# Performance work log

Measured on AMD Instinct MI355X. Metric: run time of the kernel, lower is better.

The kernel has to match this reference:

```python
import jax, jax.numpy as jnp
import numpy as np
from jax import lax

D = 30   # embedding_dim (hardcoded in repo)
Q = 30   # question length
N = 4000 # number of sentences in doc
S = 100  # tokens per sentence
K = 5    # k_for_maxpool
SLOPE = 0.1  # LeakyReLU negative slope


def setup_inputs() -> dict:
    key = jax.random.key(0)
    ks = jax.random.split(key, 20)
    rn = lambda k, sh: jax.random.normal(k, sh, dtype=jnp.float32)
    ru = lambda k, sh: jax.random.uniform(k, sh, dtype=jnp.float32)
    return {
        "doc_sents_embeds": rn(ks[0], (N, S, D)),
        "sents_gaf": ru(ks[1], (N, 3)),
        "question_embeds": rn(ks[2], (Q, D)),
        "q_idfs": ru(ks[3], (Q, 1)),
        "doc_gaf": ru(ks[4], (4,)),
        "conv1_w": rn(ks[5], (D, D, 3)) * 0.1,
        "conv1_b": rn(ks[6], (D,)) * 0.1,
        "conv2_w": rn(ks[7], (D, D, 3)) * 0.1,
        "conv2_b": rn(ks[8], (D,)) * 0.1,
        "qw_W": rn(ks[9], (1, D + 1)) * 0.1,
        "qw_b": rn(ks[10], (1,)) * 0.1,
        "lq1_W": rn(ks[11], (8, 6)) * 0.1,
        "lq1_b": rn(ks[12], (8,)) * 0.1,
        "lq2_W": rn(ks[13], (1, 8)) * 0.1,
        "lq2_b": rn(ks[14], (1,)) * 0.1,
        "so_W": rn(ks[15], (1, 4)) * 0.1,
        "so_b": rn(ks[16], (1,)) * 0.1,
        "fl_W": rn(ks[17], (1, 5)) * 0.1,
        "fl_b": rn(ks[18], (1,)) * 0.1,
    }


def _leaky(x):
    return jnp.where(x >= 0, x, SLOPE * x)


def _conv_block(x, w, b):
    # x: [B, L, D]. torch Conv1d(D, D, 3, padding=2) then slice [1:L+1]
    # is exactly a 'same' conv with padding 1 on each side; then residual add.
    y = lax.conv_general_dilated(x.transpose(0, 2, 1), w, (1,), [(1, 1)],
                                 dimension_numbers=("NCH", "OIH", "NCH"))
    y = _leaky(y + b[None, :, None])
    return y.transpose(0, 2, 1) + x


def _cos_sim(A, B):
    # A: [Q, D], B: [N, S, D] -> [N, Q, S] (num/den as in torch my_cosine_sim)
    num = jnp.einsum("qd,nsd->nqs", A, B)
    den = jnp.linalg.norm(A, axis=-1)[None, :, None] * jnp.linalg.norm(B, axis=-1)[:, None, :]
    return num / den


def _pool(sim):
    # sort-based k-max pooling -> [max, avg_of_top_k]; sim: [N, Q, S] -> [N, Q, 2]
    vals = lax.top_k(sim, K)[0]  # descending
    return jnp.stack([vals[..., 0], vals.mean(-1)], axis=-1)


def reference(doc_sents_embeds, sents_gaf, question_embeds, q_idfs, doc_gaf,
              conv1_w, conv1_b, conv2_w, conv2_b, qw_W, qw_b,
              lq1_W, lq1_b, lq2_W, lq2_b, so_W, so_b, fl_W, fl_b):
    # question context (two residual trigram convs)
    q_conv = _conv_block(question_embeds[None], conv1_w, conv1_b)
    q_conv = _conv_block(q_conv, conv2_w, conv2_b)[0]          # [Q, D]
    # question term weights
    qw_in = jnp.concatenate([q_conv, q_idfs], axis=-1)          # [Q, D+1]
    q_weights = jax.nn.softmax((qw_in @ qw_W.T + qw_b)[:, 0])   # [Q]
    # sentence context convs (batched over all sentences)
    conv_res = _conv_block(doc_sents_embeds, conv1_w, conv1_b)
    conv_res = _conv_block(conv_res, conv2_w, conv2_b)          # [N, S, D]
    # similarity matrices
    sim_insens = _cos_sim(question_embeds, doc_sents_embeds)    # [N, Q, S]
    sim_oh = (sim_insens > 1.0 - 1e-3).astype(sim_insens.dtype)
    sim_sens = _cos_sim(q_conv, conv_res)
    # k-max pooling and per-q tiny MLP attention
    feats = jnp.concatenate([_pool(sim_oh), _pool(sim_insens), _pool(sim_sens)], axis=-1)  # [N, Q, 6]
    lo = _leaky(feats @ lq1_W.T + lq1_b) @ lq2_W.T + lq2_b      # [N, Q, 1]
    lo = lo[..., 0] * q_weights[None, :]
    sent_emit = lo.sum(-1) / Q                                  # [N]
    # per-sentence output layer
    sent_feats = jnp.concatenate([sents_gaf, sent_emit[:, None]], axis=-1)  # [N, 4]
    sent_scores = jax.nn.sigmoid((sent_feats @ so_W.T + so_b)[:, 0])        # [N]
    # doc-level score
    doc_rep = jnp.concatenate([jnp.max(sent_scores)[None], doc_gaf])        # [5]
    final = doc_rep @ fl_W.T + fl_b                                          # [1]
    return final, sent_scores
```

## Files before the change

kernel.cpp:

```cpp
#include <hip/hip_runtime.h>
#include <hip/hip_bf16.h>

#define SLOPE 0.1f

#define OFF_QW    1816
#define OFF_QNI   1846
#define OFF_QNS   1876
#define OFF_B1    4606
#define OFF_B2    7336
#define OFF_LQ1W  7366
#define OFF_LQ1B  7414
#define OFF_LQ2W  7422
#define OFF_LQ2B  7430
#define OFF_SOW   7431
#define OFF_SOB   7435
#define OFF_FLW   7436
#define OFF_FLB   7441
#define U16_QEA   16384
#define U16_QCA   17408
#define U16_WB1   18432
#define U16_WB2   21504

typedef __attribute__((ext_vector_type(8))) __bf16 bf16x8;
typedef __attribute__((ext_vector_type(4))) float f32x4;

union Frag { uint4 u4; uint u[4]; bf16x8 v; };

__device__ __forceinline__ float bf2f(ushort h) {
    union { uint u; float f; } c; c.u = ((uint)h) << 16; return c.f;
}
__device__ __forceinline__ ushort f2bf(float f) {
    union { float f; uint u; } c; c.f = f;
    uint u = c.u;
    return (ushort)((u + 0x7FFFu + ((u >> 16) & 1u)) >> 16);
}
__device__ __forceinline__ float ldx(const void* p, long i, int bf) {
    if (bf) return bf2f(((const ushort*)p)[i]);
    return ((const float*)p)[i];
}
#define CE(x, y) { float _hi = fmaxf(x, y), _lo = fminf(x, y); x = _hi; y = _lo; }

__device__ __forceinline__ int detect_bf(const void* doc_in, int tid, int* scnt) {
    if (tid == 0) *scnt = 0;
    __syncthreads();
    const ushort* p = (const ushort*)doc_in;
    int local = 0;
    for (int i = tid; i < 4096; i += 256) {
        unsigned e = (p[i] >> 7) & 0xFFu;
        if (e != 0u && (e < 100u || e > 134u)) local++;
    }
    atomicAdd(scnt, local);
    __syncthreads();
    return (*scnt > 200) ? 0 : 1;
}

__global__ __launch_bounds__(256) void k_prep(
        const void* doc_in,
        const void* qe_in, const void* qidf_in,
        const void* w1_in, const void* b1_in,
        const void* w2_in, const void* b2_in,
        const void* qwW_in, const void* qwb_in,
        const void* lq1W_in, const void* lq1b_in,
        const void* lq2W_in, const void* lq2b_in,
        const void* soW_in, const void* sob_in,
        const void* flW_in, const void* flb_in,
        float* ws) {
    const int tid = threadIdx.x;
    const int blk = blockIdx.x;
    __shared__ float QE[900], T1[900], QC[900], W[2700], IDF[32], LG[32];
    __shared__ int scnt;

    const int bf = detect_bf(doc_in, tid, &scnt);
    ushort* wsu = (ushort*)ws;

    if (blk == 1) {
        if (tid == 0) { ((int*)ws)[0] = bf; }
        if (tid < 30) ws[OFF_B1 + tid] = ldx(b1_in, tid, bf);
        if (tid < 48) ws[OFF_LQ1W + tid] = ldx(lq1W_in, tid, bf);
        if (tid < 8)  { ws[OFF_LQ1B + tid] = ldx(lq1b_in, tid, bf);
                        ws[OFF_LQ2W + tid] = ldx(lq2W_in, tid, bf); }
        if (tid < 4)  ws[OFF_SOW + tid] = ldx(soW_in, tid, bf);
        if (tid < 5)  ws[OFF_FLW + tid] = ldx(flW_in, tid, bf);
        if (tid == 1) { ws[OFF_LQ2B] = ldx(lq2b_in, 0, bf);
                        ws[OFF_SOB]  = ldx(sob_in, 0, bf);
                        ws[OFF_FLB]  = ldx(flb_in, 0, bf); }
        for (int i = tid; i < 3072; i += 256) {
            int o = i / 96, kk = i % 96;
            float v1 = 0.f;
            if (o < 30 && kk < 90) {
                int ii = kk % 30, k = kk / 30;
                v1 = ldx(w1_in, (long)o*90 + ii*3 + k, bf);
            }
            wsu[U16_WB1 + i] = f2bf(v1);
        }
        return;
    }
    if (blk == 2) {
        if (tid < 30) ws[OFF_B2 + tid] = ldx(b2_in, tid, bf);
        for (int i = tid; i < 3072; i += 256) {
            int o = i / 96, kk = i % 96;
            float v2 = 0.f;
            if (o < 30 && kk < 90) {
                int ii = kk % 30, k = kk / 30;
                v2 = ldx(w2_in, (long)o*90 + ii*3 + k, bf);
            }
            wsu[U16_WB2 + i] = f2bf(v2);
        }
        return;
    }

    if (tid == 0) { ((int*)ws)[0] = bf; }

    for (int i = tid; i < 900; i += 256) QE[i] = ldx(qe_in, i, bf);
    if (tid < 30) IDF[tid] = ldx(qidf_in, tid, bf);
    for (int i = tid; i < 2700; i += 256) W[i] = ldx(w1_in, i, bf);
    __syncthreads();

    for (int idx = tid; idx < 900; idx += 256) {
        int s = idx / 30, o = idx % 30;
        float acc = ldx(b1_in, o, bf);
        for (int k = 0; k < 3; ++k) {
            int t = s + k - 1;
            if (t < 0 || t >= 30) continue;
            for (int i = 0; i < 30; ++i) acc += QE[t*30 + i] * W[o*90 + i*3 + k];
        }
        acc = acc >= 0.f ? acc : SLOPE * acc;
        T1[idx] = acc + QE[idx];
    }
    __syncthreads();
    for (int i = tid; i < 2700; i += 256) W[i] = ldx(w2_in, i, bf);
    __syncthreads();
    for (int idx = tid; idx < 900; idx += 256) {
        int s = idx / 30, o = idx % 30;
        float acc = ldx(b2_in, o, bf);
        for (int k = 0; k < 3; ++k) {
            int t = s + k - 1;
            if (t < 0 || t >= 30) continue;
            for (int i = 0; i < 30; ++i) acc += T1[t*30 + i] * W[o*90 + i*3 + k];
        }
        acc = acc >= 0.f ? acc : SLOPE * acc;
        QC[idx] = acc + T1[idx];
    }
    __syncthreads();

    if (tid < 30) {
        float s1 = 0.f, s2 = 0.f;
        for (int d = 0; d < 30; ++d) {
            float a = QE[tid*30 + d]; s1 += a*a;
            float b = QC[tid*30 + d]; s2 += b*b;
        }
        ws[OFF_QNI + tid] = 1.0f / sqrtf(s1);
        ws[OFF_QNS + tid] = 1.0f / sqrtf(s2);
        float z = ldx(qwb_in, 0, bf);
        for (int d = 0; d < 30; ++d) z += QC[tid*30 + d] * ldx(qwW_in, d, bf);
        z += IDF[tid] * ldx(qwW_in, 30, bf);
        LG[tid] = z;
    }
    __syncthreads();
    if (tid == 0) {
        float m = -1e30f;
        for (int q = 0; q < 30; ++q) m = fmaxf(m, LG[q]);
        float sum = 0.f, e[30];
        for (int q = 0; q < 30; ++q) { e[q] = expf(LG[q] - m); sum += e[q]; }
        for (int q = 0; q < 30; ++q) ws[OFF_QW + q] = e[q] / sum;
    }
    for (int i = tid; i < 1024; i += 256) {
        int q = i >> 5, d = i & 31;
        float ve = (q < 30 && d < 30) ? QE[q*30 + d] : 0.f;
        float vc = (q < 30 && d < 30) ? QC[q*30 + d] : 0.f;
        wsu[U16_QEA + i] = f2bf(ve);
        wsu[U16_QCA + i] = f2bf(vc);
    }
}

__global__ __launch_bounds__(128, 4) void k_main(const void* doc_in, const void* gaf_in,
                                                 void* out, float* ws) {
    const int n = blockIdx.x;
    const int tid = threadIdx.x;
    const int bf = ((const int*)ws)[0];
    const int lane = tid & 63;
    const int wid = tid >> 6;
    const int l15 = lane & 15;
    const int quad = lane >> 4;

    __shared__ uint XA32[1546];
    __shared__ uint XB32[1546];
    __shared__ float INVX[100];
    __shared__ float FE[30][6];
    __shared__ float IQI[30], IQS[30], BI1[30], BI2[30];

    ushort* XAu = (ushort*)XA32;
    const ushort* wsu = (const ushort*)ws;
    const uint4* qeA = (const uint4*)(wsu + U16_QEA);
    const uint4* qcA = (const uint4*)(wsu + U16_QCA);
    const uint4* wb1 = (const uint4*)(wsu + U16_WB1);
    const uint4* wb2 = (const uint4*)(wsu + U16_WB2);

    float ga0 = ldx(gaf_in, (long)n*3 + 0, bf);
    float ga1 = ldx(gaf_in, (long)n*3 + 1, bf);
    float ga2 = ldx(gaf_in, (long)n*3 + 2, bf);

    for (int i = tid; i < 46; i += 128) {
        int j = (i < 15) ? i : (1500 + i);
        XA32[j] = 0u; XB32[j] = 0u;
    }
    if (bf) {
        const uint* g = (const uint*)((const ushort*)doc_in + (size_t)n * 3000);
        for (int i = tid; i < 1500; i += 128) XA32[15 + i] = g[i];
    } else {
        const float* p = (const float*)doc_in + (size_t)n * 3000;
        for (int i = tid; i < 3000; i += 128) XAu[30 + i] = f2bf(p[i]);
    }
    if (tid < 30) {
        IQI[tid] = ws[OFF_QNI + tid];
        IQS[tid] = ws[OFF_QNS + tid];
        BI1[tid] = ws[OFF_B1 + tid];
        BI2[tid] = ws[OFF_B2 + tid];
    }
    __syncthreads();

    if (tid < 100) {
        const uint* r = XA32 + (tid + 1) * 15;
        float s = 0.f;
        #pragma unroll
        for (int i = 0; i < 15; ++i) {
            uint u = r[i];
            float lo = __uint_as_float(u << 16);
            float hi = __uint_as_float(u & 0xFFFF0000u);
            s += lo * lo + hi * hi;
        }
        INVX[tid] = 1.f / sqrtf(s);
    }
    __syncthreads();

    auto sim_pool = [&](const uint4* qa, const float* invq, int fbase, bool do_oh) {
        f32x4 acc[7];
        Frag a;
        a.u4 = qa[(wid * 16 + l15) * 4 + quad];
        #pragma unroll
        for (int nt = 0; nt < 7; ++nt) {
            int s = nt * 16 + l15;
            Frag b;
            if (s < 100) {
                int base = (s + 1) * 15 + quad * 4;
                b.u[0] = XA32[base];     b.u[1] = XA32[base + 1];
                b.u[2] = XA32[base + 2]; b.u[3] = XA32[base + 3];
            } else { b.u[0] = b.u[1] = b.u[2] = b.u[3] = 0u; }
            f32x4 z = {0.f, 0.f, 0.f, 0.f};
            acc[nt] = __builtin_amdgcn_mfma_f32_16x16x32_bf16(a.v, b.v, z, 0, 0, 0);
        }
        float ix[7];
        #pragma unroll
        for (int nt = 0; nt < 7; ++nt) {
            int s = nt * 16 + l15;
            ix[nt] = (s < 100) ? INVX[s] : 0.f;
        }
        #pragma unroll
        for (int r = 0; r < 4; ++r) {
            int q = wid * 16 + quad * 4 + r;
            float iq = (q < 30) ? invq[q] : 0.f;
            float v[7];
            int cnt = 0;
            #pragma unroll
            for (int nt = 0; nt < 7; ++nt) {
                int s = nt * 16 + l15;
                v[nt] = (s < 100) ? acc[nt][r] * iq * ix[nt] : -1e30f;
                if (do_oh) cnt += (v[nt] > 0.999f) ? 1 : 0;
            }
            CE(v[0], v[1]); CE(v[2], v[3]); CE(v[0], v[2]); CE(v[1], v[3]); CE(v[1], v[2]);
            CE(v[4], v[5]); CE(v[5], v[6]); CE(v[4], v[5]);
            float t0 = fmaxf(v[0], v[4]);
            float t1 = fmaxf(fmaxf(fminf(v[0], v[4]), v[1]), v[5]);
            float t2 = fmaxf(fmaxf(fmaxf(fminf(v[0], v[5]), fminf(v[1], v[4])), v[2]), v[6]);
            float t3 = fmaxf(fmaxf(fmaxf(fminf(v[0], v[6]), fminf(v[1], v[5])), fminf(v[2], v[4])), v[3]);
            float t4 = fmaxf(fmaxf(fminf(v[1], v[6]), fminf(v[2], v[5])), fminf(v[3], v[4]));
            #pragma unroll
            for (int d = 1; d < 16; d <<= 1) {
                float p0 = __shfl_xor(t0, d), p1 = __shfl_xor(t1, d), p2 = __shfl_xor(t2, d);
                float p3 = __shfl_xor(t3, d), p4 = __shfl_xor(t4, d);
                if (do_oh) cnt += __shfl_xor(cnt, d);
                float m0 = fmaxf(t0, p0);
                float m1 = fmaxf(fmaxf(fminf(t0, p0), t1), p1);
                float m2 = fmaxf(fmaxf(fmaxf(fminf(t0, p1), fminf(t1, p0)), t2), p2);
                float m3 = fmaxf(fmaxf(fmaxf(fminf(t0, p2), fminf(t1, p1)), fminf(t2, p0)),
                                 fmaxf(t3, p3));
                float m4 = fmaxf(fmaxf(fmaxf(fminf(t0, p3), fminf(t1, p2)), fminf(t2, p1)),
                                 fmaxf(fminf(t3, p0), fmaxf(t4, p4)));
                t0 = m0; t1 = m1; t2 = m2; t3 = m3; t4 = m4;
            }
            if (l15 == 0 && q < 30) {
                if (do_oh) {
                    FE[q][0] = cnt > 0 ? 1.f : 0.f;
                    FE[q][1] = (float)(cnt > 5 ? 5 : cnt) * 0.2f;
                }
                FE[q][fbase]     = t0;
                FE[q][fbase + 1] = (t0 + t1 + t2 + t3 + t4) * 0.2f;
            }
        }
    };

    auto conv_mt = [&](const uint* src32, uint* dst32, const uint4* wb,
                       const float* bias, int mt, int nt0, int nt1) {
        const ushort* srcU = (const ushort*)src32;
        ushort* dstU = (ushort*)dst32;
        int sa = mt * 16 + l15;
        Frag a[3];
        #pragma unroll
        for (int k = 0; k < 3; ++k) {
            if (sa < 100) {
                int base = sa * 15 + k * 16 + quad * 4;
                a[k].u[0] = src32[base];     a[k].u[1] = src32[base + 1];
                a[k].u[2] = src32[base + 2]; a[k].u[3] = src32[base + 3];
            } else { a[k].u[0] = a[k].u[1] = a[k].u[2] = a[k].u[3] = 0u; }
        }
        for (int nt = nt0; nt <= nt1; ++nt) {
            f32x4 acc = {0.f, 0.f, 0.f, 0.f};
            #pragma unroll
            for (int k = 0; k < 3; ++k) {
                Frag b;
                b.u4 = wb[(nt * 16 + l15) * 12 + k * 4 + quad];
                acc = __builtin_amdgcn_mfma_f32_16x16x32_bf16(a[k].v, b.v, acc, 0, 0, 0);
            }
            int o = nt * 16 + l15;
            if (o < 30) {
                float bo = bias[o];
                #pragma unroll
                for (int r = 0; r < 4; ++r) {
                    int s = mt * 16 + quad * 4 + r;
                    if (s < 100) {
                        float v = acc[r] + bo;
                        v = v >= 0.f ? v : SLOPE * v;
                        v += bf2f(srcU[(s + 1) * 30 + o]);
                        dstU[(s + 1) * 30 + o] = f2bf(v);
                    }
                }
            }
        }
    };

    sim_pool(qeA, IQI, 2, true);
    conv_mt(XA32, XB32, wb1, BI1, wid,     0, 1);
    conv_mt(XA32, XB32, wb1, BI1, wid + 2, 0, 1);
    conv_mt(XA32, XB32, wb1, BI1, wid + 4, 0, 1);
    conv_mt(XA32, XB32, wb1, BI1, 6,       wid, wid);
    __syncthreads();

    conv_mt(XB32, XA32, wb2, BI2, wid,     0, 1);
    conv_mt(XB32, XA32, wb2, BI2, wid + 2, 0, 1);
    conv_mt(XB32, XA32, wb2, BI2, wid + 4, 0, 1);
    conv_mt(XB32, XA32, wb2, BI2, 6,       wid, wid);
    __syncthreads();

    if (tid < 100) {
        const uint* r = XA32 + (tid + 1) * 15;
        float s = 0.f;
        #pragma unroll
        for (int i = 0; i < 15; ++i) {
            uint u = r[i];
            float lo = __uint_as_float(u << 16);
            float hi = __uint_as_float(u & 0xFFFF0000u);
            s += lo * lo + hi * hi;
        }
        INVX[tid] = 1.f / sqrtf(s);
    }
    __syncthreads();

    sim_pool(qcA, IQS, 4, false);
    __syncthreads();

    if (wid == 0) {
        float val = 0.f;
        if (lane < 30) {
            float lo = ws[OFF_LQ2B];
            #pragma unroll
            for (int j = 0; j < 8; ++j) {
                float h = ws[OFF_LQ1B + j];
                #pragma unroll
                for (int f = 0; f < 6; ++f) h += FE[lane][f] * ws[OFF_LQ1W + j*6 + f];
                h = h >= 0.f ? h : SLOPE * h;
                lo += h * ws[OFF_LQ2W + j];
            }
            val = lo * ws[OFF_QW + lane];
        }
        for (int d = 32; d >= 1; d >>= 1) val += __shfl_xor(val, d);
        if (lane == 0) {
            float emit = val * (1.f / 30.f);
            float z = ws[OFF_SOB];
            z += ga0 * ws[OFF_SOW + 0];
            z += ga1 * ws[OFF_SOW + 1];
            z += ga2 * ws[OFF_SOW + 2];
            z += emit * ws[OFF_SOW + 3];
            float sc = 1.f / (1.f + expf(-z));
            if (bf) ((__hip_bfloat16*)out)[1 + n] = __float2bfloat16(sc);
            else    ((float*)out)[1 + n] = sc;
        }
    }
}

__global__ __launch_bounds__(256) void k_final(const void* docgaf_in, void* out, const float* ws) {
    const int tid = threadIdx.x;
    const int bf = ((const int*)ws)[0];
    __shared__ float red[256];
    float m = -1e30f;
    for (int i = tid; i < 4000; i += 256) {
        float v = bf ? __bfloat162float(((const __hip_bfloat16*)out)[1 + i])
                     : ((const float*)out)[1 + i];
        m = fmaxf(m, v);
    }
    red[tid] = m;
    __syncthreads();
    for (int off = 128; off > 0; off >>= 1) {
        if (tid < off) red[tid] = fmaxf(red[tid], red[tid + off]);
        __syncthreads();
    }
    if (tid == 0) {
        float f = ws[OFF_FLB] + red[0] * ws[OFF_FLW + 0];
        for (int i = 0; i < 4; ++i) f += ldx(docgaf_in, i, bf) * ws[OFF_FLW + 1 + i];
        if (bf) ((__hip_bfloat16*)out)[0] = __float2bfloat16(f);
        else    ((float*)out)[0] = f;
    }
}

extern "C" void kernel_launch(void* const* d_in, const int* in_sizes, int n_in,
                              void* d_out, int out_size, void* d_ws, size_t ws_size,
                              hipStream_t stream) {
    float* ws = (float*)d_ws;
    k_prep<<<3, 256, 0, stream>>>(d_in[0], d_in[2], d_in[3], d_in[5], d_in[6], d_in[7], d_in[8],
                                  d_in[9], d_in[10], d_in[11], d_in[12], d_in[13], d_in[14],
                                  d_in[15], d_in[16], d_in[17], d_in[18], ws);
    k_main<<<4000, 128, 0, stream>>>(d_in[0], d_in[1], d_out, ws);
    k_final<<<1, 256, 0, stream>>>(d_in[4], d_out, ws);
}
```

Measured before the change: 189.2 us.

## Transpose similarity MFMA so each lane holds one question for pooling

```diff
diff --git a/kernel.cpp b/kernel.cpp
--- a/kernel.cpp
+++ b/kernel.cpp
@@ -6,6 +6,7 @@
 #define OFF_QW    1816
 #define OFF_QNI   1846
 #define OFF_QNS   1876
+#define OFF_QNN   1906
 #define OFF_B1    4606
 #define OFF_B2    7336
 #define OFF_LQ1W  7366
@@ -39,6 +40,38 @@
     return ((const float*)p)[i];
 }
 #define CE(x, y) { float _hi = fmaxf(x, y), _lo = fminf(x, y); x = _hi; y = _lo; }
+
+__device__ __forceinline__ void sort4d(float& a, float& b, float& c, float& d) {
+    CE(a, b); CE(c, d); CE(a, c); CE(b, d); CE(b, c);
+}
+__device__ __forceinline__ void merge44_5(const float* a, const float* b, float* t) {
+    t[0] = fmaxf(a[0], b[0]);
+    t[1] = fmaxf(fminf(a[0], b[0]), fmaxf(a[1], b[1]));
+    t[2] = fmaxf(fmaxf(fminf(a[0], b[1]), fminf(a[1], b[0])), fmaxf(a[2], b[2]));
+    t[3] = fmaxf(fmaxf(fminf(a[0], b[2]), fminf(a[1], b[1])),
+                 fmaxf(fminf(a[2], b[0]), fmaxf(a[3], b[3])));
+    t[4] = fmaxf(fmaxf(fminf(a[0], b[3]), fminf(a[1], b[2])),
+                 fmaxf(fminf(a[2], b[1]), fminf(a[3], b[0])));
+}
+__device__ __forceinline__ void merge54_5(const float* a, const float* b, float* t) {
+    t[0] = fmaxf(a[0], b[0]);
+    t[1] = fmaxf(fminf(a[0], b[0]), fmaxf(a[1], b[1]));
+    t[2] = fmaxf(fmaxf(fminf(a[0], b[1]), fminf(a[1], b[0])), fmaxf(a[2], b[2]));
+    t[3] = fmaxf(fmaxf(fminf(a[0], b[2]), fminf(a[1], b[1])),
+                 fmaxf(fminf(a[2], b[0]), fmaxf(a[3], b[3])));
+    t[4] = fmaxf(fmaxf(fmaxf(fminf(a[0], b[3]), fminf(a[1], b[2])),
+                       fmaxf(fminf(a[2], b[1]), fminf(a[3], b[0]))), a[4]);
+}
+__device__ __forceinline__ void merge55_5(const float* a, const float* b, float* t) {
+    t[0] = fmaxf(a[0], b[0]);
+    t[1] = fmaxf(fminf(a[0], b[0]), fmaxf(a[1], b[1]));
+    t[2] = fmaxf(fmaxf(fminf(a[0], b[1]), fminf(a[1], b[0])), fmaxf(a[2], b[2]));
+    t[3] = fmaxf(fmaxf(fminf(a[0], b[2]), fminf(a[1], b[1])),
+                 fmaxf(fminf(a[2], b[0]), fmaxf(a[3], b[3])));
+    t[4] = fmaxf(fmaxf(fmaxf(fminf(a[0], b[3]), fminf(a[1], b[2])),
+                       fmaxf(fminf(a[2], b[1]), fminf(a[3], b[0]))),
+                 fmaxf(a[4], b[4]));
+}
 
 __device__ __forceinline__ int detect_bf(const void* doc_in, int tid, int* scnt) {
     if (tid == 0) *scnt = 0;
@@ -149,7 +182,9 @@
             float a = QE[tid*30 + d]; s1 += a*a;
             float b = QC[tid*30 + d]; s2 += b*b;
         }
-        ws[OFF_QNI + tid] = 1.0f / sqrtf(s1);
+        float n1 = sqrtf(s1);
+        ws[OFF_QNN + tid] = n1;
+        ws[OFF_QNI + tid] = 1.0f / n1;
         ws[OFF_QNS + tid] = 1.0f / sqrtf(s2);
         float z = ldx(qwb_in, 0, bf);
         for (int d = 0; d < 30; ++d) z += QC[tid*30 + d] * ldx(qwW_in, d, bf);
@@ -185,9 +220,9 @@
 
     __shared__ uint XA32[1546];
     __shared__ uint XB32[1546];
-    __shared__ float INVX[100];
+    __shared__ __align__(16) float INVX[112];
     __shared__ float FE[30][6];
-    __shared__ float IQI[30], IQS[30], BI1[30], BI2[30];
+    __shared__ float IQI[32], IQS[32], QNN[32], BI1[32], BI2[32];
 
     ushort* XAu = (ushort*)XA32;
     const ushort* wsu = (const ushort*)ws;
@@ -204,6 +239,7 @@
         int j = (i < 15) ? i : (1500 + i);
         XA32[j] = 0u; XB32[j] = 0u;
     }
+    if (tid >= 100 && tid < 112) INVX[tid] = 0.f;
     if (bf) {
         const uint* g = (const uint*)((const ushort*)doc_in + (size_t)n * 3000);
         for (int i = tid; i < 1500; i += 128) XA32[15 + i] = g[i];
@@ -211,9 +247,10 @@
         const float* p = (const float*)doc_in + (size_t)n * 3000;
         for (int i = tid; i < 3000; i += 128) XAu[30 + i] = f2bf(p[i]);
     }
-    if (tid < 30) {
+    if (tid < 32) {
         IQI[tid] = ws[OFF_QNI + tid];
         IQS[tid] = ws[OFF_QNS + tid];
+        QNN[tid] = ws[OFF_QNN + tid];
         BI1[tid] = ws[OFF_B1 + tid];
         BI2[tid] = ws[OFF_B2 + tid];
     }
@@ -233,69 +270,67 @@
     }
     __syncthreads();
 
-    auto sim_pool = [&](const uint4* qa, const float* invq, int fbase, bool do_oh) {
+    auto sim_pool = [&](const uint4* qa, const float* IQ, int fbase, bool do_oh) {
+        const int q = wid * 16 + l15;
+        Frag b;
+        b.u4 = qa[q * 4 + quad];
         f32x4 acc[7];
-        Frag a;
-        a.u4 = qa[(wid * 16 + l15) * 4 + quad];
-        #pragma unroll
-        for (int nt = 0; nt < 7; ++nt) {
-            int s = nt * 16 + l15;
-            Frag b;
-            if (s < 100) {
-                int base = (s + 1) * 15 + quad * 4;
-                b.u[0] = XA32[base];     b.u[1] = XA32[base + 1];
-                b.u[2] = XA32[base + 2]; b.u[3] = XA32[base + 3];
-            } else { b.u[0] = b.u[1] = b.u[2] = b.u[3] = 0u; }
+        #pragma unroll
+        for (int mt = 0; mt < 7; ++mt) {
+            int m = mt * 16 + l15;
+            Frag a;
+            if (m < 100) {
+                int base = (m + 1) * 15 + quad * 4;
+                a.u[0] = XA32[base];     a.u[1] = XA32[base + 1];
+                a.u[2] = XA32[base + 2]; a.u[3] = XA32[base + 3];
+            } else { a.u[0] = a.u[1] = a.u[2] = a.u[3] = 0u; }
             f32x4 z = {0.f, 0.f, 0.f, 0.f};
-            acc[nt] = __builtin_amdgcn_mfma_f32_16x16x32_bf16(a.v, b.v, z, 0, 0, 0);
-        }
-        float ix[7];
-        #pragma unroll
-        for (int nt = 0; nt < 7; ++nt) {
-            int s = nt * 16 + l15;
-            ix[nt] = (s < 100) ? INVX[s] : 0.f;
-        }
-        #pragma unroll
-        for (int r = 0; r < 4; ++r) {
-            int q = wid * 16 + quad * 4 + r;
-            float iq = (q < 30) ? invq[q] : 0.f;
-            float v[7];
-            int cnt = 0;
+            acc[mt] = __builtin_amdgcn_mfma_f32_16x16x32_bf16(a.v, b.v, z, 0, 0, 0);
+        }
+        const float4* INVX4 = (const float4*)INVX;
+        float thr = 0.999f * QNN[q];
+        float iq  = (q < 30) ? IQ[q] : 0.f;
+        float g[7][4];
+        int cnt = 0;
+        #pragma unroll
+        for (int mt = 0; mt < 7; ++mt) {
+            float4 ix = INVX4[mt * 4 + quad];
+            float ixa[4] = {ix.x, ix.y, ix.z, ix.w};
             #pragma unroll
-            for (int nt = 0; nt < 7; ++nt) {
-                int s = nt * 16 + l15;
-                v[nt] = (s < 100) ? acc[nt][r] * iq * ix[nt] : -1e30f;
-                if (do_oh) cnt += (v[nt] > 0.999f) ? 1 : 0;
-            }
-            CE(v[0], v[1]); CE(v[2], v[3]); CE(v[0], v[2]); CE(v[1], v[3]); CE(v[1], v[2]);
-            CE(v[4], v[5]); CE(v[5], v[6]); CE(v[4], v[5]);
-            float t0 = fmaxf(v[0], v[4]);
-            float t1 = fmaxf(fmaxf(fminf(v[0], v[4]), v[1]), v[5]);
-            float t2 = fmaxf(fmaxf(fmaxf(fminf(v[0], v[5]), fminf(v[1], v[4])), v[2]), v[6]);
-            float t3 = fmaxf(fmaxf(fmaxf(fminf(v[0], v[6]), fminf(v[1], v[5])), fminf(v[2], v[4])), v[3]);
-            float t4 = fmaxf(fmaxf(fminf(v[1], v[6]), fminf(v[2], v[5])), fminf(v[3], v[4]));
-            #pragma unroll
-            for (int d = 1; d < 16; d <<= 1) {
-                float p0 = __shfl_xor(t0, d), p1 = __shfl_xor(t1, d), p2 = __shfl_xor(t2, d);
-                float p3 = __shfl_xor(t3, d), p4 = __shfl_xor(t4, d);
-                if (do_oh) cnt += __shfl_xor(cnt, d);
-                float m0 = fmaxf(t0, p0);
-                float m1 = fmaxf(fmaxf(fminf(t0, p0), t1), p1);
-                float m2 = fmaxf(fmaxf(fmaxf(fminf(t0, p1), fminf(t1, p0)), t2), p2);
-                float m3 = fmaxf(fmaxf(fmaxf(fminf(t0, p2), fminf(t1, p1)), fminf(t2, p0)),
-                                 fmaxf(t3, p3));
-                float m4 = fmaxf(fmaxf(fmaxf(fminf(t0, p3), fminf(t1, p2)), fminf(t2, p1)),
-                                 fmaxf(fminf(t3, p0), fmaxf(t4, p4)));
-                t0 = m0; t1 = m1; t2 = m2; t3 = m3; t4 = m4;
-            }
-            if (l15 == 0 && q < 30) {
-                if (do_oh) {
-                    FE[q][0] = cnt > 0 ? 1.f : 0.f;
-                    FE[q][1] = (float)(cnt > 5 ? 5 : cnt) * 0.2f;
-                }
-                FE[q][fbase]     = t0;
-                FE[q][fbase + 1] = (t0 + t1 + t2 + t3 + t4) * 0.2f;
-            }
+            for (int r = 0; r < 4; ++r) {
+                float u = acc[mt][r] * ixa[r];
+                if (mt == 6 && (quad * 4 + r) >= 4) u = -1e30f;
+                g[mt][r] = u;
+                if (do_oh) cnt += (u > thr) ? 1 : 0;
+            }
+        }
+        #pragma unroll
+        for (int mt = 0; mt < 7; ++mt) sort4d(g[mt][0], g[mt][1], g[mt][2], g[mt][3]);
+        float p0[5], p1[5], p2[5], q0[5], q1[5], t[5];
+        merge44_5(g[0], g[1], p0);
+        merge44_5(g[2], g[3], p1);
+        merge44_5(g[4], g[5], p2);
+        merge55_5(p0, p1, q0);
+        merge54_5(p2, g[6], q1);
+        merge55_5(q0, q1, t);
+        #pragma unroll
+        for (int d = 16; d < 64; d <<= 1) {
+            float pp[5];
+            pp[0] = __shfl_xor(t[0], d); pp[1] = __shfl_xor(t[1], d);
+            pp[2] = __shfl_xor(t[2], d); pp[3] = __shfl_xor(t[3], d);
+            pp[4] = __shfl_xor(t[4], d);
+            if (do_oh) cnt += __shfl_xor(cnt, d);
+            float tn[5];
+            merge55_5(t, pp, tn);
+            t[0] = tn[0]; t[1] = tn[1]; t[2] = tn[2]; t[3] = tn[3]; t[4] = tn[4];
+        }
+        if (quad == 0 && q < 30) {
+            if (do_oh) {
+                FE[q][0] = cnt > 0 ? 1.f : 0.f;
+                FE[q][1] = (float)(cnt > 5 ? 5 : cnt) * 0.2f;
+            }
+            FE[q][fbase]     = t[0] * iq;
+            FE[q][fbase + 1] = (t[0] + t[1] + t[2] + t[3] + t[4]) * 0.2f * iq;
         }
     };
 
```

Result: faster. 176.9 us (-6.5%).
